# Kernel optimization log

Measured on AMD Instinct MI355X. Metric: run time of the kernel, lower is better.

Reference implementation:

```python
import jax, jax.numpy as jnp
import numpy as np


def setup_inputs() -> dict:
    key = jax.random.key(0)
    kq, kk, kv = jax.random.split(key, 3)
    n, m, d, v = 4096, 4096, 1024, 1024
    Q = jax.random.normal(kq, (n, d), dtype=jnp.float32)
    K = jax.random.normal(kk, (m, d), dtype=jnp.float32)
    V = jax.random.normal(kv, (m, v), dtype=jnp.float32)
    return {"Q": Q, "K": K, "V": V}


def reference(Q, K, V):
    d = K.shape[-1]
    scale = d ** (-0.5)
    logits = jnp.matmul(Q, K.T)                      # [n, m]
    # Faithful to source: softmax over dim=1 (keys), THEN scaled by d**-0.5
    scores = jax.nn.softmax(logits, axis=1) * scale  # [n, m]
    return jnp.matmul(scores, V)                     # [n, v]
```

## Files before the change

### kernel.cpp

```cpp
#include <hip/hip_runtime.h>
#include <hip/hip_bf16.h>

typedef _Float16 f16x8 __attribute__((ext_vector_type(8)));
typedef _Float16 f16x4 __attribute__((ext_vector_type(4)));
typedef float f32x4 __attribute__((ext_vector_type(4)));

__device__ __forceinline__ void async_ld16(_Float16* lds, const _Float16* g) {
    __builtin_amdgcn_global_load_lds(
        (const __attribute__((address_space(1))) void*)g,
        (__attribute__((address_space(3))) void*)lds, 16, 0, 0);
}

__global__ __launch_bounds__(512, 2) void gemm_bt256(
    const _Float16* __restrict__ A,
    const _Float16* __restrict__ B,
    float* __restrict__ C,
    int M, int N, int K, int Ks)
{
    __shared__ _Float16 Asm[2][256 * 32];
    __shared__ _Float16 Bsm[2][256 * 32];

    const int tid  = threadIdx.x;
    const int w    = tid >> 6;
    const int lane = tid & 63;
    const int l16  = lane & 15;
    const int quad = lane >> 4;
    const int wm   = w >> 2;
    const int wn   = w & 3;

    const int gx = gridDim.x, gy = gridDim.y;
    const int total = gx * gy * (int)gridDim.z;
    int lid = (int)blockIdx.x + gx * ((int)blockIdx.y + gy * (int)blockIdx.z);
    {
        const int q = total >> 3, r = total & 7;
        const int xcd = lid & 7, i = lid >> 3;
        lid = (xcd < r ? xcd * (q + 1) : r * (q + 1) + (xcd - r) * q) + i;
    }
    const int bx = lid % gx;
    const int by = (lid / gx) % gy;
    const int bz = lid / (gx * gy);

    const int row0 = by * 256;
    const int col0 = bx * 256;

    const _Float16* Ab = A + (size_t)row0 * K + (size_t)bz * Ks;
    const _Float16* Bb = B + (size_t)col0 * K + (size_t)bz * Ks;

    const int srow = lane >> 2;
    const int sch  = (lane & 3) * 8;
    const _Float16* pa = Ab + (size_t)(w * 32 + srow) * K + sch;
    const _Float16* pb = Bb + (size_t)(w * 32 + srow) * K + sch;
    const size_t r16 = (size_t)16 * K;

    f32x4 acc[8][4] = {};
    const int NT = Ks >> 5;

    {
        _Float16* as = &Asm[0][0] + w * 1024;
        _Float16* bs = &Bsm[0][0] + w * 1024;
        async_ld16(as,       pa);
        async_ld16(as + 512, pa + r16);
        async_ld16(bs,       pb);
        async_ld16(bs + 512, pb + r16);
    }
    __syncthreads();

    const int aoff = (wm * 16 + l16) * 32 + quad * 8;
    const int boff = (wn * 16 + l16) * 32 + quad * 8;

    for (int t = 0; t < NT; ++t) {
        const int buf = t & 1;

        if (t + 1 < NT) {
            const int kc = (t + 1) * 32;
            _Float16* as = &Asm[buf ^ 1][0] + w * 1024;
            _Float16* bs = &Bsm[buf ^ 1][0] + w * 1024;
            async_ld16(as,       pa + kc);
            async_ld16(as + 512, pa + kc + r16);
            async_ld16(bs,       pb + kc);
            async_ld16(bs + 512, pb + kc + r16);
        }

        const _Float16* abuf = &Asm[buf][0];
        const _Float16* bbuf = &Bsm[buf][0];

        f16x8 af[8], bf[4];
        #pragma unroll
        for (int i = 0; i < 8; ++i)
            af[i] = *(const f16x8*)(abuf + (i >> 2) * 4096 + (i & 3) * 1024 + aoff);
        #pragma unroll
        for (int j = 0; j < 4; ++j)
            bf[j] = *(const f16x8*)(bbuf + (j >> 1) * 4096 + (j & 1) * 2048 + boff);

        #pragma unroll
        for (int i = 0; i < 8; ++i)
            #pragma unroll
            for (int j = 0; j < 4; ++j)
                acc[i][j] = __builtin_amdgcn_mfma_f32_16x16x32_f16(af[i], bf[j], acc[i][j], 0, 0, 0);

        __syncthreads();
    }

    float* Cb = C + (size_t)bz * ((size_t)M * N);
    #pragma unroll
    for (int i = 0; i < 8; ++i) {
        const int ms = i >> 2, m = i & 3;
        const int gr = row0 + ms * 128 + m * 32 + wm * 16 + quad * 4;
        #pragma unroll
        for (int j = 0; j < 4; ++j) {
            const int ns = j >> 1, nn = j & 1;
            const int gc = col0 + ns * 128 + nn * 64 + wn * 16 + l16;
            const f32x4 v = acc[i][j];
            #pragma unroll
            for (int e = 0; e < 4; ++e)
                Cb[(size_t)(gr + e) * N + gc] = v[e];
        }
    }
}

__global__ __launch_bounds__(256) void gemm_bt(
    const _Float16* __restrict__ A,
    const _Float16* __restrict__ B,
    float* __restrict__ C,
    int M, int N, int K, int Ks)
{
    __shared__ _Float16 At[2][128 * 32];
    __shared__ _Float16 Bt[2][128 * 32];

    const int tid  = threadIdx.x;
    const int wave = tid >> 6;
    const int lane = tid & 63;

    int gx = gridDim.x, gy = gridDim.y;
    int bx = blockIdx.x, by = blockIdx.y;
    if (((gx & 7) == 0) && ((gy & 7) == 0)) {
        const int bid    = bx + gx * by;
        const int ntx    = gx >> 3;
        const int sid    = bid >> 6;
        const int within = bid & 63;
        const int sx = sid % ntx;
        const int sy = sid / ntx;
        bx = (sx << 3) + (within & 7);
        by = (sy << 3) + (within >> 3);
    }
    const int row0 = by * 128;
    const int col0 = bx * 128;

    const int wr = (wave >> 1) * 64;
    const int wc = (wave & 1) * 64;
    const int quad = lane >> 4;
    const int l16  = lane & 15;

    f32x4 acc[4][4] = {};

    const int srow  = lane >> 2;
    const int skoff = (lane & 3) * 8;
    const size_t K64 = (size_t)64 * K;

    const _Float16* Ab = A + (size_t)row0 * K + (size_t)blockIdx.z * Ks;
    const _Float16* Bb = B + (size_t)col0 * K + (size_t)blockIdx.z * Ks;
    float* Cb = C + (size_t)blockIdx.z * M * N;

    const _Float16* pa = Ab + (size_t)(wave * 16 + srow) * K + skoff;
    const _Float16* pb = Bb + (size_t)(wave * 16 + srow) * K + skoff;

    async_ld16(At[0] + wave * 512,       pa);
    async_ld16(At[0] + (wave + 4) * 512, pa + K64);
    async_ld16(Bt[0] + wave * 512,       pb);
    async_ld16(Bt[0] + (wave + 4) * 512, pb + K64);
    __syncthreads();

    int cur = 0;
    for (int k0 = 0; k0 < Ks; k0 += 32) {
        const int nxt = cur ^ 1;
        if (k0 + 32 < Ks) {
            const _Float16* qa = pa + k0 + 32;
            const _Float16* qb = pb + k0 + 32;
            async_ld16(At[nxt] + wave * 512,       qa);
            async_ld16(At[nxt] + (wave + 4) * 512, qa + K64);
            async_ld16(Bt[nxt] + wave * 512,       qb);
            async_ld16(Bt[nxt] + (wave + 4) * 512, qb + K64);
        }

        f16x8 af[4], bf[4];
        #pragma unroll
        for (int r = 0; r < 4; ++r)
            af[r] = *(const f16x8*)&At[cur][(wr + r * 16 + l16) * 32 + quad * 8];
        #pragma unroll
        for (int c = 0; c < 4; ++c)
            bf[c] = *(const f16x8*)&Bt[cur][(wc + c * 16 + l16) * 32 + quad * 8];

        #pragma unroll
        for (int r = 0; r < 4; ++r)
            #pragma unroll
            for (int c = 0; c < 4; ++c)
                acc[r][c] = __builtin_amdgcn_mfma_f32_16x16x32_f16(af[r], bf[c], acc[r][c], 0, 0, 0);

        __syncthreads();
        cur = nxt;
    }

    #pragma unroll
    for (int r = 0; r < 4; ++r) {
        const int growb = row0 + wr + r * 16 + quad * 4;
        #pragma unroll
        for (int c = 0; c < 4; ++c) {
            const int gcol = col0 + wc + c * 16 + l16;
            #pragma unroll
            for (int i = 0; i < 4; ++i)
                Cb[(size_t)(growb + i) * N + gcol] = acc[r][c][i];
        }
    }
}

__global__ __launch_bounds__(256) void softmax_rows(
    const float* __restrict__ S, _Float16* __restrict__ P, float scale)
{
    __shared__ float red[4];
    const int row = blockIdx.x;
    const int tid = threadIdx.x;
    const int wave = tid >> 6;
    const float4* Sr = (const float4*)(S + (size_t)row * 4096);

    float4 x[4];
    #pragma unroll
    for (int i = 0; i < 4; ++i) x[i] = Sr[tid + i * 256];

    float mx = -3.402823466e+38f;
    #pragma unroll
    for (int i = 0; i < 4; ++i)
        mx = fmaxf(mx, fmaxf(fmaxf(x[i].x, x[i].y), fmaxf(x[i].z, x[i].w)));
    #pragma unroll
    for (int off = 32; off > 0; off >>= 1) mx = fmaxf(mx, __shfl_down(mx, off));
    if ((tid & 63) == 0) red[wave] = mx;
    __syncthreads();
    mx = fmaxf(fmaxf(red[0], red[1]), fmaxf(red[2], red[3]));
    __syncthreads();

    float sum = 0.0f;
    #pragma unroll
    for (int i = 0; i < 4; ++i) {
        x[i].x = __expf(x[i].x - mx);
        x[i].y = __expf(x[i].y - mx);
        x[i].z = __expf(x[i].z - mx);
        x[i].w = __expf(x[i].w - mx);
        sum += x[i].x + x[i].y + x[i].z + x[i].w;
    }
    #pragma unroll
    for (int off = 32; off > 0; off >>= 1) sum += __shfl_down(sum, off);
    if ((tid & 63) == 0) red[wave] = sum;
    __syncthreads();
    sum = red[0] + red[1] + red[2] + red[3];

    const float inv = scale / sum;
    f16x4* Pr = (f16x4*)(P + (size_t)row * 4096);
    #pragma unroll
    for (int i = 0; i < 4; ++i) {
        f16x4 h;
        h.x = (_Float16)(x[i].x * inv);
        h.y = (_Float16)(x[i].y * inv);
        h.z = (_Float16)(x[i].z * inv);
        h.w = (_Float16)(x[i].w * inv);
        Pr[tid + i * 256] = h;
    }
}

__global__ __launch_bounds__(256) void cvt2_f32_f16(
    const float4* __restrict__ a, f16x4* __restrict__ da, int n4a,
    const float4* __restrict__ b, f16x4* __restrict__ db, int n4b)
{
    int i = blockIdx.x * 256 + threadIdx.x;
    const int stride = gridDim.x * 256;
    const int tot = n4a + n4b;
    for (; i < tot; i += stride) {
        const float4* s = (i < n4a) ? (a + i) : (b + (i - n4a));
        f16x4* d = (i < n4a) ? (da + i) : (db + (i - n4a));
        float4 v = *s;
        f16x4 h;
        h.x = (_Float16)v.x; h.y = (_Float16)v.y;
        h.z = (_Float16)v.z; h.w = (_Float16)v.w;
        *d = h;
    }
}

__global__ __launch_bounds__(256) void transpose_cvt(
    const float* __restrict__ V, _Float16* __restrict__ Vt, int rows, int cols)
{
    __shared__ float tile[32][33];
    const int c0 = blockIdx.x * 32;
    const int r0 = blockIdx.y * 32;
    const int tx = threadIdx.x & 31;
    const int ty = threadIdx.x >> 5;
    #pragma unroll
    for (int i = 0; i < 4; ++i)
        tile[ty * 4 + i][tx] = V[(size_t)(r0 + ty * 4 + i) * cols + c0 + tx];
    __syncthreads();
    #pragma unroll
    for (int i = 0; i < 4; ++i)
        Vt[(size_t)(c0 + ty * 4 + i) * rows + r0 + tx] = (_Float16)tile[tx][ty * 4 + i];
}

__global__ __launch_bounds__(256) void reduce2(
    const float4* __restrict__ a, const float4* __restrict__ b,
    float4* __restrict__ o, int n4)
{
    int i = blockIdx.x * 256 + threadIdx.x;
    const int stride = gridDim.x * 256;
    for (; i < n4; i += stride) {
        float4 u = a[i], v = b[i];
        float4 w;
        w.x = u.x + v.x; w.y = u.y + v.y; w.z = u.z + v.z; w.w = u.w + v.w;
        o[i] = w;
    }
}

__global__ __launch_bounds__(256) void reduce4(
    const float4* __restrict__ a, const float4* __restrict__ b,
    const float4* __restrict__ c, const float4* __restrict__ d,
    float4* __restrict__ o, int n4)
{
    int i = blockIdx.x * 256 + threadIdx.x;
    const int stride = gridDim.x * 256;
    for (; i < n4; i += stride) {
        float4 u = a[i], v = b[i], x = c[i], y = d[i];
        float4 w;
        w.x = (u.x + v.x) + (x.x + y.x);
        w.y = (u.y + v.y) + (x.y + y.y);
        w.z = (u.z + v.z) + (x.z + y.z);
        w.w = (u.w + v.w) + (x.w + y.w);
        o[i] = w;
    }
}

extern "C" void kernel_launch(void* const* d_in, const int* in_sizes, int n_in,
                              void* d_out, int out_size, void* d_ws, size_t ws_size,
                              hipStream_t stream) {
    const float* Q = (const float*)d_in[0];
    const float* K = (const float*)d_in[1];
    const float* V = (const float*)d_in[2];
    float* out = (float*)d_out;

    const int n = 4096, m = 4096, d = 1024, vdim = 1024;
    const float scale = 0.03125f;

    char* w = (char*)d_ws;
    _Float16* Qh = (_Float16*)w;
    _Float16* Kh = (_Float16*)(w + (8u << 20));
    _Float16* Vt = (_Float16*)(w + (16u << 20));
    char* rest = w + (24u << 20);
    size_t avail = ws_size > (24u << 20) ? ws_size - (24u << 20) : 0;

    int nc = 128;
    if      ((size_t)4096 * m * 6 <= avail) nc = 4096;
    else if ((size_t)2048 * m * 6 <= avail) nc = 2048;
    else if ((size_t)1024 * m * 6 <= avail) nc = 1024;
    else if ((size_t)512  * m * 6 <= avail) nc = 512;
    else if ((size_t)256  * m * 6 <= avail) nc = 256;

    float*    S = (float*)rest;
    _Float16* P = (_Float16*)(rest + (size_t)nc * m * 4);
    float* part = S;

    cvt2_f32_f16<<<dim3(2048), dim3(256), 0, stream>>>(
        (const float4*)Q, (f16x4*)Qh, n * d / 4,
        (const float4*)K, (f16x4*)Kh, m * d / 4);
    transpose_cvt<<<dim3(vdim / 32, m / 32), dim3(256), 0, stream>>>(V, Vt, m, vdim);

    if (nc >= 256) {
        for (int r0 = 0; r0 < n; r0 += nc) {
            gemm_bt256<<<dim3(m / 256, nc / 256, 1), dim3(512), 0, stream>>>(
                Qh + (size_t)r0 * d, Kh, S, nc, m, d, d);
            softmax_rows<<<dim3(nc), dim3(256), 0, stream>>>(S, P, scale);
            gemm_bt256<<<dim3(vdim / 256, nc / 256, 4), dim3(512), 0, stream>>>(
                P, Vt, part, nc, vdim, m, m / 4);
            reduce4<<<dim3(1024), dim3(256), 0, stream>>>(
                (const float4*)part,
                (const float4*)(part + (size_t)nc * vdim),
                (const float4*)(part + (size_t)2 * nc * vdim),
                (const float4*)(part + (size_t)3 * nc * vdim),
                (float4*)(out + (size_t)r0 * vdim), nc * vdim / 4);
        }
    } else {
        for (int r0 = 0; r0 < n; r0 += nc) {
            gemm_bt<<<dim3(m / 128, nc / 128, 1), dim3(256), 0, stream>>>(
                Qh + (size_t)r0 * d, Kh, S, nc, m, d, d);
            softmax_rows<<<dim3(nc), dim3(256), 0, stream>>>(S, P, scale);
            gemm_bt<<<dim3(vdim / 128, nc / 128, 2), dim3(256), 0, stream>>>(
                P, Vt, part, nc, vdim, m, m / 2);
            reduce2<<<dim3(1024), dim3(256), 0, stream>>>(
                (const float4*)part, (const float4*)(part + (size_t)nc * vdim),
                (float4*)(out + (size_t)r0 * vdim), nc * vdim / 4);
        }
    }
}
```

Before: 220.7 us.

## Pipeline 256x256 GEMM with K=64 tiles, swizzled LDS, and staged quarter-tile prefetch

The 256x256 fp16 GEMM kernel now uses a K-step of 64 with an XOR-swizzled LDS layout to avoid bank conflicts. The main loop is split into four phases, each reading half-tile fragments and issuing MFMAs at raised priority. Between phases, the next tiles' half-blocks are prefetched asynchronously two iterations ahead, with explicit vmcnt and lgkmcnt waits and raw barriers replacing __syncthreads. This aims to overlap global loads with compute and cut LDS stalls, at the cost of doubled LDS use, which may limit occupancy, and fragile hand-managed wait counts.

```diff
diff --git a/kernel.cpp b/kernel.cpp
--- a/kernel.cpp
+++ b/kernel.cpp
@@ -10,6 +10,10 @@
         (const __attribute__((address_space(1))) void*)g,
         (__attribute__((address_space(3))) void*)lds, 16, 0, 0);
 }
+
+#define VMCNT(n) asm volatile("s_waitcnt vmcnt(" #n ")" ::: "memory")
+#define LGKMCNT0 asm volatile("s_waitcnt lgkmcnt(0)" ::: "memory")
+#define BAR() __builtin_amdgcn_s_barrier()
 
 __global__ __launch_bounds__(512, 2) void gemm_bt256(
     const _Float16* __restrict__ A,
@@ -17,8 +21,8 @@
     float* __restrict__ C,
     int M, int N, int K, int Ks)
 {
-    __shared__ _Float16 Asm[2][256 * 32];
-    __shared__ _Float16 Bsm[2][256 * 32];
+    __shared__ _Float16 Asm[2][256 * 64];
+    __shared__ _Float16 Bsm[2][256 * 64];
 
     const int tid  = threadIdx.x;
     const int w    = tid >> 6;
@@ -46,59 +50,115 @@
     const _Float16* Ab = A + (size_t)row0 * K + (size_t)bz * Ks;
     const _Float16* Bb = B + (size_t)col0 * K + (size_t)bz * Ks;
 
-    const int srow = lane >> 2;
-    const int sch  = (lane & 3) * 8;
-    const _Float16* pa = Ab + (size_t)(w * 32 + srow) * K + sch;
-    const _Float16* pb = Bb + (size_t)(w * 32 + srow) * K + sch;
-    const size_t r16 = (size_t)16 * K;
+    const int lr = lane >> 3;
+    const int lc = (lane & 7) ^ lr;
+    const size_t soff  = (size_t)(w * 16 + lr) * K + lc * 8;
+    const _Float16* pa = Ab + soff;
+    const _Float16* pb = Bb + soff;
+    const size_t jstep = (size_t)8 * K;
+    const size_t hstep = (size_t)128 * K;
+
+    auto STAGE = [&](_Float16* sm, const _Float16* gsrc, int h, int kcol) {
+        _Float16* d = sm + h * 8192 + w * 1024;
+        const _Float16* s = gsrc + (size_t)h * hstep + kcol;
+        async_ld16(d,       s);
+        async_ld16(d + 512, s + jstep);
+    };
+
+    const int abase = (wm * 16 + l16) * 64;
+    const int bbase = (wn * 16 + l16) * 64;
+    const int rs0   = ((quad)     ^ (l16 & 7)) * 8;
+    const int rs1   = ((4 + quad) ^ (l16 & 7)) * 8;
+
+#define READ_A(dst, msoff)                                                     \
+    _Pragma("unroll")                                                          \
+    for (int m_ = 0; m_ < 4; ++m_) {                                           \
+        dst[m_][0] = *(const f16x8*)(abuf + (msoff) + m_ * 2048 + abase + rs0);\
+        dst[m_][1] = *(const f16x8*)(abuf + (msoff) + m_ * 2048 + abase + rs1);\
+    }
+#define READ_B(dst, nsoff)                                                     \
+    _Pragma("unroll")                                                          \
+    for (int n_ = 0; n_ < 2; ++n_) {                                           \
+        dst[n_][0] = *(const f16x8*)(bbuf + (nsoff) + n_ * 4096 + bbase + rs0);\
+        dst[n_][1] = *(const f16x8*)(bbuf + (nsoff) + n_ * 4096 + bbase + rs1);\
+    }
+#define MFMA4x2(accrow, afrag, bfrag, bcol)                                    \
+    _Pragma("unroll")                                                          \
+    for (int m_ = 0; m_ < 4; ++m_)                                             \
+      _Pragma("unroll")                                                        \
+      for (int n_ = 0; n_ < 2; ++n_) {                                         \
+        acc[(accrow) + m_][(bcol) + n_] =                                      \
+            __builtin_amdgcn_mfma_f32_16x16x32_f16(                            \
+                afrag[m_][0], bfrag[n_][0], acc[(accrow) + m_][(bcol) + n_],   \
+                0, 0, 0);                                                      \
+        acc[(accrow) + m_][(bcol) + n_] =                                      \
+            __builtin_amdgcn_mfma_f32_16x16x32_f16(                            \
+                afrag[m_][1], bfrag[n_][1], acc[(accrow) + m_][(bcol) + n_],   \
+                0, 0, 0);                                                      \
+      }
 
     f32x4 acc[8][4] = {};
-    const int NT = Ks >> 5;
-
-    {
-        _Float16* as = &Asm[0][0] + w * 1024;
-        _Float16* bs = &Bsm[0][0] + w * 1024;
-        async_ld16(as,       pa);
-        async_ld16(as + 512, pa + r16);
-        async_ld16(bs,       pb);
-        async_ld16(bs + 512, pb + r16);
-    }
-    __syncthreads();
-
-    const int aoff = (wm * 16 + l16) * 32 + quad * 8;
-    const int boff = (wn * 16 + l16) * 32 + quad * 8;
+    const int NT = Ks >> 6;
+
+    STAGE(&Asm[0][0], pa, 0, 0);
+    STAGE(&Bsm[0][0], pb, 0, 0);
+    STAGE(&Bsm[0][0], pb, 1, 0);
+    STAGE(&Asm[0][0], pa, 1, 0);
+    if (NT > 1) {
+        STAGE(&Asm[1][0], pa, 0, 64);
+        STAGE(&Bsm[1][0], pb, 0, 64);
+        STAGE(&Bsm[1][0], pb, 1, 64);
+        VMCNT(6);
+    } else {
+        VMCNT(0);
+    }
+    BAR();
 
     for (int t = 0; t < NT; ++t) {
         const int buf = t & 1;
-
-        if (t + 1 < NT) {
-            const int kc = (t + 1) * 32;
-            _Float16* as = &Asm[buf ^ 1][0] + w * 1024;
-            _Float16* bs = &Bsm[buf ^ 1][0] + w * 1024;
-            async_ld16(as,       pa + kc);
-            async_ld16(as + 512, pa + kc + r16);
-            async_ld16(bs,       pb + kc);
-            async_ld16(bs + 512, pb + kc + r16);
-        }
-
         const _Float16* abuf = &Asm[buf][0];
         const _Float16* bbuf = &Bsm[buf][0];
-
-        f16x8 af[8], bf[4];
-        #pragma unroll
-        for (int i = 0; i < 8; ++i)
-            af[i] = *(const f16x8*)(abuf + (i >> 2) * 4096 + (i & 3) * 1024 + aoff);
-        #pragma unroll
-        for (int j = 0; j < 4; ++j)
-            bf[j] = *(const f16x8*)(bbuf + (j >> 1) * 4096 + (j & 1) * 2048 + boff);
-
-        #pragma unroll
-        for (int i = 0; i < 8; ++i)
-            #pragma unroll
-            for (int j = 0; j < 4; ++j)
-                acc[i][j] = __builtin_amdgcn_mfma_f32_16x16x32_f16(af[i], bf[j], acc[i][j], 0, 0, 0);
-
-        __syncthreads();
+        _Float16* const acur = &Asm[buf][0];
+        _Float16* const bcur = &Bsm[buf][0];
+        _Float16* const anxt = &Asm[buf ^ 1][0];
+
+        f16x8 alo[4][2], ahi[4][2], blo[2][2], bhi[2][2];
+
+        READ_A(alo, 0);
+        READ_B(blo, 0);
+        if (t + 1 < NT) STAGE(anxt, pa, 1, (t + 1) * 64);
+        BAR();
+        LGKMCNT0;
+        __builtin_amdgcn_s_setprio(1);
+        MFMA4x2(0, alo, blo, 0);
+        __builtin_amdgcn_s_setprio(0);
+        BAR();
+
+        READ_B(bhi, 8192);
+        if (t + 2 < NT) STAGE(acur, pa, 0, (t + 2) * 64);
+        BAR();
+        LGKMCNT0;
+        __builtin_amdgcn_s_setprio(1);
+        MFMA4x2(0, alo, bhi, 2);
+        __builtin_amdgcn_s_setprio(0);
+        BAR();
+
+        READ_A(ahi, 8192);
+        if (t + 2 < NT) STAGE(bcur, pb, 0, (t + 2) * 64);
+        BAR();
+        LGKMCNT0;
+        __builtin_amdgcn_s_setprio(1);
+        MFMA4x2(4, ahi, bhi, 2);
+        __builtin_amdgcn_s_setprio(0);
+        BAR();
+
+        if (t + 2 < NT) STAGE(bcur, pb, 1, (t + 2) * 64);
+        BAR();
+        __builtin_amdgcn_s_setprio(1);
+        MFMA4x2(4, ahi, blo, 0);
+        __builtin_amdgcn_s_setprio(0);
+        if (t + 2 < NT) { VMCNT(6); } else { VMCNT(0); }
+        BAR();
     }
 
     float* Cb = C + (size_t)bz * ((size_t)M * N);
@@ -116,6 +176,9 @@
                 Cb[(size_t)(gr + e) * N + gc] = v[e];
         }
     }
+#undef READ_A
+#undef READ_B
+#undef MFMA4x2
 }
 
 __global__ __launch_bounds__(256) void gemm_bt(
```

Measured after the change: 199.0 us. 1.11x faster.
